# Kernel optimization log

Measured on AMD Instinct MI355X. Metric: run time of the kernel, lower is better.

## Reference

```python
import jax, jax.numpy as jnp
import numpy as np

# Module constants (from init_kwargs)
B, NIN, NOUT = 128, 1024, 1024
G_OFF, G_ON, K_V = 0.001, 0.003, 0.5


def setup_inputs() -> dict:
    key = jax.random.key(0)
    k1, k2, k3 = jax.random.split(key, 3)
    stdv = 1.0 / np.sqrt(NIN)
    x = jax.random.normal(k1, (B, NIN), dtype=jnp.float32)
    # NonNeg-constrained weights, RandomNormal(mean=0.5, std=1/sqrt(in))
    w_pos = jnp.abs(0.5 + stdv * jax.random.normal(k2, (NIN, NOUT), dtype=jnp.float32))
    w_neg = jnp.abs(0.5 + stdv * jax.random.normal(k3, (NIN, NOUT), dtype=jnp.float32))
    b_pos = jnp.full((NOUT,), 0.5, dtype=jnp.float32)
    b_neg = jnp.full((NOUT,), 0.5, dtype=jnp.float32)
    return {"x": x, "w_pos": w_pos, "w_neg": w_neg, "b_pos": b_pos, "b_neg": b_neg}


def reference(x, w_pos, w_neg, b_pos, b_neg):
    # combine_weights(): append bias row, interleave pos/neg columns -> [in+1, 2*out]
    comb_pos = jnp.concatenate([w_pos, b_pos[None, :]], axis=0)  # [in+1, out]
    comb_neg = jnp.concatenate([w_neg, b_neg[None, :]], axis=0)  # [in+1, out]
    weights = jnp.stack([comb_pos, comb_neg], axis=-1).reshape(NIN + 1, 2 * NOUT)

    # append ones column for bias input; scale to voltages
    ones = jnp.ones((x.shape[0], 1), dtype=x.dtype)
    voltages = K_V * jnp.concatenate([x, ones], axis=1)  # [B, in+1]

    # double_weights_to_conductances: linear map of weights into [G_off, G_on]
    max_w = jnp.max(weights)
    k_cond = (G_ON - G_OFF) / max_w
    conductances = k_cond * weights + G_OFF  # [in+1, 2*out]

    # eval path: expand-multiply-reduce == matmul (same math, fused here)
    currents = voltages @ conductances  # [B, 2*out]

    # differential pair readout and rescale back to weight units
    total_currents = currents[:, 0::2] - currents[:, 1::2]  # [B, out]
    y_disturbed = total_currents / (K_V * k_cond)
    return y_disturbed
```

## Files before the change

### kernel.cpp

```cpp
#include <hip/hip_runtime.h>


#define NB   128
#define NIN  1024
#define NOUT 1024

#define BM   64
#define BN   32
#define KC   128
#define XPAD 132

__global__ __launch_bounds__(256, 2) void memr_fc(
    const float* __restrict__ x,  const float* __restrict__ wp,
    const float* __restrict__ wn, const float* __restrict__ bp,
    const float* __restrict__ bn, float* __restrict__ out)
{
    __shared__ float xs[BM * XPAD];
    __shared__ float wd[KC * BN];

    const int t  = threadIdx.x;
    const int o0 = blockIdx.x * BN;
    const int b0 = blockIdx.y * BM;
    const int k0 = blockIdx.z * KC;

    #pragma unroll
    for (int r = 0; r < 8; ++r) {
        const int f4 = r * 256 + t;
        const int b  = f4 >> 5;
        const int q  = f4 & 31;
        const float4 v = *(const float4*)&x[(size_t)(b0 + b) * NIN + k0 + q * 4];
        *(float4*)&xs[b * XPAD + q * 4] = v;
    }
    #pragma unroll
    for (int r = 0; r < 4; ++r) {
        const int f4 = r * 256 + t;
        const int k  = f4 >> 3;
        const int q  = f4 & 7;
        const size_t g = (size_t)(k0 + k) * NOUT + o0 + q * 4;
        const float4 p = *(const float4*)&wp[g];
        const float4 n = *(const float4*)&wn[g];
        float4 d;
        d.x = p.x - n.x; d.y = p.y - n.y; d.z = p.z - n.z; d.w = p.w - n.w;
        *(float4*)&wd[k * BN + q * 4] = d;
    }
    __syncthreads();

    const int tx = t & 7;
    const int ty = t >> 3;

    float acc[2][4] = {{0.f,0.f,0.f,0.f},{0.f,0.f,0.f,0.f}};

    const float* xr0 = &xs[(ty * 2 + 0) * XPAD];
    const float* xr1 = &xs[(ty * 2 + 1) * XPAD];
    const float* wr  = &wd[tx * 4];

    #pragma unroll 8
    for (int k = 0; k < KC; ++k) {
        const float4 w4 = *(const float4*)&wr[k * BN];
        const float x0 = xr0[k];
        const float x1 = xr1[k];
        acc[0][0] += x0 * w4.x; acc[0][1] += x0 * w4.y;
        acc[0][2] += x0 * w4.z; acc[0][3] += x0 * w4.w;
        acc[1][0] += x1 * w4.x; acc[1][1] += x1 * w4.y;
        acc[1][2] += x1 * w4.z; acc[1][3] += x1 * w4.w;
    }

    float bias[4] = {0.f, 0.f, 0.f, 0.f};
    if (blockIdx.z == 0) {
        #pragma unroll
        for (int j = 0; j < 4; ++j) {
            const int o = o0 + tx * 4 + j;
            bias[j] = bp[o] - bn[o];
        }
    }

    #pragma unroll
    for (int i = 0; i < 2; ++i) {
        const int b = b0 + ty * 2 + i;
        #pragma unroll
        for (int j = 0; j < 4; ++j)
            atomicAdd(&out[(size_t)b * NOUT + o0 + tx * 4 + j], acc[i][j] + bias[j]);
    }
}

extern "C" void kernel_launch(void* const* d_in, const int* in_sizes, int n_in,
                              void* d_out, int out_size, void* d_ws, size_t ws_size,
                              hipStream_t stream)
{
    const float* x  = (const float*)d_in[0];
    const float* wp = (const float*)d_in[1];
    const float* wn = (const float*)d_in[2];
    const float* bp = (const float*)d_in[3];
    const float* bn = (const float*)d_in[4];
    float* out = (float*)d_out;

    hipMemsetAsync(out, 0, (size_t)NB * NOUT * sizeof(float), stream);

    dim3 grid(NOUT / BN, NB / BM, NIN / KC);
    memr_fc<<<grid, 256, 0, stream>>>(x, wp, wn, bp, bn, out);
}
```

Measured before the change: 85.49 us.

## Replace atomic split-K with workspace partials and a separate reduce kernel

Drops the memset and the atomicAdd accumulation. Each block now writes its split-K partial tile to a workspace, and a second kernel sums the 16 partials and adds the bias. Tiles are retiled so each block covers all 128 batch rows with 8x4 outputs per thread, which raises register reuse and removes weight re-reads across batch blocks. In exchange it adds an 8 MB workspace write and read plus a second launch, and the grid shrinks to 512 blocks of 128 threads.

```diff
diff --git a/kernel.cpp b/kernel.cpp
--- a/kernel.cpp
+++ b/kernel.cpp
@@ -5,82 +5,94 @@
 #define NIN  1024
 #define NOUT 1024
 
-#define BM   64
-#define BN   32
-#define KC   128
-#define XPAD 132
+#define OT   32
+#define KC   64
+#define NKS  (NIN / KC)
+#define XP   65
 
-__global__ __launch_bounds__(256, 2) void memr_fc(
+__global__ __launch_bounds__(128) void memr_partial(
     const float* __restrict__ x,  const float* __restrict__ wp,
-    const float* __restrict__ wn, const float* __restrict__ bp,
-    const float* __restrict__ bn, float* __restrict__ out)
+    const float* __restrict__ wn, float* __restrict__ ws)
 {
-    __shared__ float xs[BM * XPAD];
-    __shared__ float wd[KC * BN];
+    __shared__ float xs[NB * XP];
+    __shared__ float wd[KC * OT];
 
     const int t  = threadIdx.x;
-    const int o0 = blockIdx.x * BN;
-    const int b0 = blockIdx.y * BM;
-    const int k0 = blockIdx.z * KC;
+    const int o0 = blockIdx.x * OT;
+    const int ks = blockIdx.y;
+    const int k0 = ks * KC;
 
     #pragma unroll
-    for (int r = 0; r < 8; ++r) {
-        const int f4 = r * 256 + t;
-        const int b  = f4 >> 5;
-        const int q  = f4 & 31;
-        const float4 v = *(const float4*)&x[(size_t)(b0 + b) * NIN + k0 + q * 4];
-        *(float4*)&xs[b * XPAD + q * 4] = v;
+    for (int r = 0; r < 16; ++r) {
+        const int f4 = r * 128 + t;
+        const int b  = f4 >> 4;
+        const int q  = f4 & 15;
+        const float4 v = *(const float4*)&x[(size_t)b * NIN + k0 + q * 4];
+        float* d = &xs[b * XP + q * 4];
+        d[0] = v.x; d[1] = v.y; d[2] = v.z; d[3] = v.w;
     }
     #pragma unroll
     for (int r = 0; r < 4; ++r) {
-        const int f4 = r * 256 + t;
+        const int f4 = r * 128 + t;
         const int k  = f4 >> 3;
         const int q  = f4 & 7;
         const size_t g = (size_t)(k0 + k) * NOUT + o0 + q * 4;
         const float4 p = *(const float4*)&wp[g];
         const float4 n = *(const float4*)&wn[g];
-        float4 d;
-        d.x = p.x - n.x; d.y = p.y - n.y; d.z = p.z - n.z; d.w = p.w - n.w;
-        *(float4*)&wd[k * BN + q * 4] = d;
+        float4 d4;
+        d4.x = p.x - n.x; d4.y = p.y - n.y; d4.z = p.z - n.z; d4.w = p.w - n.w;
+        *(float4*)&wd[k * OT + q * 4] = d4;
     }
     __syncthreads();
 
     const int tx = t & 7;
     const int ty = t >> 3;
 
-    float acc[2][4] = {{0.f,0.f,0.f,0.f},{0.f,0.f,0.f,0.f}};
+    float acc[8][4];
+    #pragma unroll
+    for (int i = 0; i < 8; ++i)
+        #pragma unroll
+        for (int j = 0; j < 4; ++j) acc[i][j] = 0.f;
 
-    const float* xr0 = &xs[(ty * 2 + 0) * XPAD];
-    const float* xr1 = &xs[(ty * 2 + 1) * XPAD];
-    const float* wr  = &wd[tx * 4];
+    const float* xr = &xs[ty * 8 * XP];
+    const float* wr = &wd[tx * 4];
 
-    #pragma unroll 8
+    #pragma unroll 4
     for (int k = 0; k < KC; ++k) {
-        const float4 w4 = *(const float4*)&wr[k * BN];
-        const float x0 = xr0[k];
-        const float x1 = xr1[k];
-        acc[0][0] += x0 * w4.x; acc[0][1] += x0 * w4.y;
-        acc[0][2] += x0 * w4.z; acc[0][3] += x0 * w4.w;
-        acc[1][0] += x1 * w4.x; acc[1][1] += x1 * w4.y;
-        acc[1][2] += x1 * w4.z; acc[1][3] += x1 * w4.w;
-    }
-
-    float bias[4] = {0.f, 0.f, 0.f, 0.f};
-    if (blockIdx.z == 0) {
+        const float4 w4 = *(const float4*)&wr[k * OT];
+        float xv[8];
         #pragma unroll
-        for (int j = 0; j < 4; ++j) {
-            const int o = o0 + tx * 4 + j;
-            bias[j] = bp[o] - bn[o];
+        for (int i = 0; i < 8; ++i) xv[i] = xr[i * XP + k];
+        #pragma unroll
+        for (int i = 0; i < 8; ++i) {
+            acc[i][0] += xv[i] * w4.x;
+            acc[i][1] += xv[i] * w4.y;
+            acc[i][2] += xv[i] * w4.z;
+            acc[i][3] += xv[i] * w4.w;
         }
     }
 
+    float* wsb = ws + (size_t)ks * NB * NOUT;
     #pragma unroll
-    for (int i = 0; i < 2; ++i) {
-        const int b = b0 + ty * 2 + i;
-        #pragma unroll
-        for (int j = 0; j < 4; ++j)
-            atomicAdd(&out[(size_t)b * NOUT + o0 + tx * 4 + j], acc[i][j] + bias[j]);
+    for (int i = 0; i < 8; ++i) {
+        const int b = ty * 8 + i;
+        float4 v;
+        v.x = acc[i][0]; v.y = acc[i][1]; v.z = acc[i][2]; v.w = acc[i][3];
+        *(float4*)&wsb[(size_t)b * NOUT + o0 + tx * 4] = v;
     }
+}
+
+__global__ __launch_bounds__(256) void memr_reduce(
+    const float* __restrict__ ws, const float* __restrict__ bp,
+    const float* __restrict__ bn, float* __restrict__ out)
+{
+    const int g = blockIdx.x * 256 + threadIdx.x;
+    const int o = g & (NOUT - 1);
+    float s = bp[o] - bn[o];
+    #pragma unroll
+    for (int ks = 0; ks < NKS; ++ks)
+        s += ws[(size_t)ks * NB * NOUT + g];
+    out[g] = s;
 }
 
 extern "C" void kernel_launch(void* const* d_in, const int* in_sizes, int n_in,
@@ -93,9 +105,9 @@
     const float* bp = (const float*)d_in[3];
     const float* bn = (const float*)d_in[4];
     float* out = (float*)d_out;
+    float* ws  = (float*)d_ws;
 
-    hipMemsetAsync(out, 0, (size_t)NB * NOUT * sizeof(float), stream);
-
-    dim3 grid(NOUT / BN, NB / BM, NIN / KC);
-    memr_fc<<<grid, 256, 0, stream>>>(x, wp, wn, bp, bn, out);
+    dim3 g1(NOUT / OT, NKS);
+    memr_partial<<<g1, 128, 0, stream>>>(x, wp, wn, ws);
+    memr_reduce<<<NB * NOUT / 256, 256, 0, stream>>>(ws, bp, bn, out);
 }
```

Result: faster. 78.01 us (-8.7%).
